# Performance work log

Hardware: AMD Instinct MI355X
Metric: run time of the kernel (lower is better)

Reference implementation:

```python
import jax, jax.numpy as jnp
import numpy as np

B, T, D = 16, 512, 256          # batch, seq_len, d_model (= num features = num graph nodes N)
H, MC, K, DE, DH = 4, 4, 3, 10, 128
GS, SS, AS = 4, 6, 4            # global/sector/asset regime states
TAU = 0.5
STEPS = 3                       # diffusion steps
HID = max(64, D)
DEC_H = max(64, D // 2)


def setup_inputs() -> dict:
    key = jax.random.key(0)
    ks = iter(jax.random.split(key, 64))

    def nrm(shape, s=0.02):
        return (s * jax.random.normal(next(ks), shape)).astype(jnp.float32)

    z = lambda *s: jnp.zeros(s, jnp.float32)
    o = lambda *s: jnp.ones(s, jnp.float32)
    p = dict(
        x=jax.random.normal(next(ks), (B, T, D), dtype=jnp.float32),
        # hierarchical regime controller
        gW1=nrm((D, HID)), gb1=z(HID), g_ln_w=o(HID), g_ln_b=z(HID),
        gW2=nrm((HID, GS)), gb2=z(GS),
        sW1=nrm((D, HID)), sb1=z(HID), sW2=nrm((HID, D * SS)), sb2=z(D * SS),
        aW1=nrm((D, HID)), ab1=z(HID), aW2=nrm((HID, D * AS)), ab2=z(D * AS),
        global_prior=z(GS), sector_prior=z(SS), asset_prior=z(AS),
        g2f=nrm((GS, D)),
        sector_emb=jax.random.normal(next(ks), (SS, D), dtype=jnp.float32),
        asset_emb=jax.random.normal(next(ks), (AS, D), dtype=jnp.float32),
        # bidirectional temporal scan (BI-Mamba stand-in)
        decay_f=nrm((D,), 1.0), decay_b=nrm((D,), 1.0),
        tW=nrm((D, D)), tb=z(D),
        # Bayesian MAGAC + diffusion graph prior
        psi=nrm((H, D, DE), 0.1), log_sigma=jnp.full((H,), -2.0, jnp.float32),
        step_logits=jnp.linspace(-1.0, 0.5, STEPS).astype(jnp.float32),
        noise_scale=jnp.full((STEPS,), 0.05, jnp.float32),
        Wk=nrm((K + 1, T, DH)),
        mean_w=nrm((DH,)), mean_b=z(), lv_w=nrm((DH,)), lv_b=z(),
        # risk-aware decoder
        dW1=nrm((D, DEC_H)), db1=z(DEC_H), d_ln_w=o(DEC_H), d_ln_b=z(DEC_H),
        mW=nrm((DEC_H,)), mb=z(), lvW=nrm((DEC_H,)), lvb=z(),
        cW=nrm((DEC_H,)), cb=z(),
    )
    return p


def _ln(h, w, b):
    m = h.mean(-1, keepdims=True)
    v = h.var(-1, keepdims=True)  # biased, matches torch LayerNorm
    return (h - m) / jnp.sqrt(v + 1e-5) * w + b


def _gelu(h):
    return jax.nn.gelu(h, approximate=False)


def _gumbel_softmax(k, logits):
    u = jax.random.uniform(k, logits.shape, minval=1e-6, maxval=1.0 - 1e-6)
    g = -jnp.log(-jnp.log(u))
    return jax.nn.softmax((logits + g) / TAU, axis=-1)


def _fwd(x, gW1, gb1, g_ln_w, g_ln_b, gW2, gb2, sW1, sb1, sW2, sb2,
         aW1, ab1, aW2, ab2, global_prior, sector_prior, asset_prior,
         g2f, sector_emb, asset_emb, decay_f, decay_b, tW, tb,
         psi, log_sigma, step_logits, noise_scale, Wk,
         mean_w, mean_b, lv_w, lv_b,
         dW1, db1, d_ln_w, d_ln_b, mW, mb, lvW, lvb, cW, cb):
    rk = jax.random.key(42)
    k_g, k_s, k_a, k_eps, k_diff = jax.random.split(rk, 5)

    # ---- hierarchical regime controller ----
    seq_mean = x.mean(1)                               # (B, D)
    diff_summary = (x[:, 1:] - x[:, :-1]).mean(1)      # (B, D)
    g_logits = _gelu(_ln(seq_mean @ gW1 + gb1, g_ln_w, g_ln_b)) @ gW2 + gb2
    s_logits = (_gelu(seq_mean @ sW1 + sb1) @ sW2 + sb2).reshape(B, D, SS)
    a_logits = (_gelu(diff_summary @ aW1 + ab1) @ aW2 + ab2).reshape(B, D, AS)
    g_probs = _gumbel_softmax(k_g, g_logits)
    s_probs = _gumbel_softmax(k_s, s_logits)
    a_probs = _gumbel_softmax(k_a, a_logits)
    global_gate = g_probs @ g2f                                   # (B, D)
    # diagonal of einsum('bfs,sd->bfd') == einsum('bfs,sf->bf')
    sector_gate = jnp.einsum('bfs,sf->bf', s_probs, sector_emb)
    asset_gate = jnp.einsum('bfs,sf->bf', a_probs, asset_emb)
    feature_gate = jax.nn.sigmoid(global_gate + sector_gate + asset_gate)
    gated_x = x * feature_gate[:, None, :]

    # ---- bidirectional temporal EMA scan (BI-Mamba stand-in) ----
    af = jax.nn.sigmoid(decay_f)
    abk = jax.nn.sigmoid(decay_b)
    xs = gated_x.transpose(1, 0, 2)                    # (T, B, D)

    def ema(a):
        def step(h, xt):
            h = a * h + (1.0 - a) * xt
            return h, h
        return step

    _, hf = jax.lax.scan(ema(af), jnp.zeros_like(xs[0]), xs)
    _, hb = jax.lax.scan(ema(abk), jnp.zeros_like(xs[0]), xs[::-1])
    temporal = (hf + hb[::-1]).transpose(1, 0, 2) @ tW + tb       # (B, T, D)
    node_major = temporal.transpose(0, 2, 1)                      # (B, N=D, T)

    # ---- Bayesian adjacency sampling (MC samples per head) ----
    logits = jnp.einsum('hne,hme->hnm', psi, psi) / jnp.sqrt(jnp.float32(DE))
    sigma = jnp.exp(log_sigma)                                    # (H,)
    eps = jax.random.normal(k_eps, (MC, H, D, D))
    A = jax.nn.softmax(logits[None] + sigma[None, :, None, None] * eps, axis=-1)

    # ---- diffusion refinement guided by regime features ----
    ctx = feature_gate.mean(0)
    ctx = ctx / (jnp.linalg.norm(ctx) + 1e-6)
    outer = ctx[:, None] * ctx[None, :]
    outer = outer / jnp.maximum(outer.sum(-1, keepdims=True), 1e-6)
    dkeys = jax.random.split(k_diff, STEPS)
    for s in range(STEPS):                             # fixed small loop, vectorized over (MC,H)
        alpha = jax.nn.sigmoid(step_logits[s])
        noise = noise_scale[s] * jax.random.normal(dkeys[s], A.shape)
        A = alpha * A + (1.0 - alpha) * outer + noise
        A = 0.5 * (A + jnp.swapaxes(A, -1, -2))
        A = jax.nn.softmax(A, axis=-1)

    # ---- K-hop graph conv, averaged over MC samples and heads ----
    Z = jnp.einsum('bnt,td->bnd', node_major, Wk[0])[None, None]  # hop 0
    P = jnp.broadcast_to(node_major, (MC, H, B, D, T))
    for k in range(1, K + 1):
        P = jnp.einsum('mhnp,mhbpt->mhbnt', A, P)
        Z = Z + jnp.einsum('mhbnt,td->mhbnd', P, Wk[k])
    Z = Z.mean((0, 1))                                            # (B, N, DH)
    graph_mean = Z @ mean_w + mean_b                              # (B, N)
    graph_logvar = Z @ lv_w + lv_b                                # (B, N)

    # ---- risk-aware decoder ----
    feat = _ln(_gelu(graph_mean @ dW1 + db1), d_ln_w, d_ln_b)     # (B, DEC_H)
    mean = feat @ mW + mb
    dec_logvar = feat @ lvW + lvb
    _cvar = jax.nn.sigmoid(feat @ cW + cb)  # auxiliary head (not in returned output)
    var = jnp.exp(dec_logvar) + jnp.exp(graph_logvar).sum(1)
    log_var = jnp.log(var)
    return jnp.stack([mean, log_var], axis=-1)                    # (B, 2)


def reference(x, gW1, gb1, g_ln_w, g_ln_b, gW2, gb2, sW1, sb1, sW2, sb2,
              aW1, ab1, aW2, ab2, global_prior, sector_prior, asset_prior,
              g2f, sector_emb, asset_emb, decay_f, decay_b, tW, tb,
              psi, log_sigma, step_logits, noise_scale, Wk,
              mean_w, mean_b, lv_w, lv_b,
              dW1, db1, d_ln_w, d_ln_b, mW, mb, lvW, lvb, cW, cb):
    return _fwd(x, gW1, gb1, g_ln_w, g_ln_b, gW2, gb2, sW1, sb1, sW2, sb2,
                aW1, ab1, aW2, ab2, global_prior, sector_prior, asset_prior,
                g2f, sector_emb, asset_emb, decay_f, decay_b, tW, tb,
                psi, log_sigma, step_logits, noise_scale, Wk,
                mean_w, mean_b, lv_w, lv_b,
                dW1, db1, d_ln_w, d_ln_b, mW, mb, lvW, lvb, cW, cb)
```

## Files before the change

### kernel.cpp

```cpp
#include <hip/hip_runtime.h>
#include <stdint.h>

#define PARTITIONABLE 1

namespace {

struct TFPair { uint32_t a, b; };

__host__ __device__ constexpr uint32_t rotl32(uint32_t x, int d) {
  return (x << d) | (x >> (32 - d));
}

__host__ __device__ constexpr TFPair tf2x32(uint32_t k0, uint32_t k1,
                                            uint32_t x0, uint32_t x1) {
  uint32_t k2 = k0 ^ k1 ^ 0x1BD11BDAu;
  x0 += k0; x1 += k1;
  x0 += x1; x1 = rotl32(x1, 13); x1 ^= x0;
  x0 += x1; x1 = rotl32(x1, 15); x1 ^= x0;
  x0 += x1; x1 = rotl32(x1, 26); x1 ^= x0;
  x0 += x1; x1 = rotl32(x1, 6);  x1 ^= x0;
  x0 += k1; x1 += k2 + 1u;
  x0 += x1; x1 = rotl32(x1, 17); x1 ^= x0;
  x0 += x1; x1 = rotl32(x1, 29); x1 ^= x0;
  x0 += x1; x1 = rotl32(x1, 16); x1 ^= x0;
  x0 += x1; x1 = rotl32(x1, 24); x1 ^= x0;
  x0 += k2; x1 += k0 + 2u;
  x0 += x1; x1 = rotl32(x1, 13); x1 ^= x0;
  x0 += x1; x1 = rotl32(x1, 15); x1 ^= x0;
  x0 += x1; x1 = rotl32(x1, 26); x1 ^= x0;
  x0 += x1; x1 = rotl32(x1, 6);  x1 ^= x0;
  x0 += k0; x1 += k1 + 3u;
  x0 += x1; x1 = rotl32(x1, 17); x1 ^= x0;
  x0 += x1; x1 = rotl32(x1, 29); x1 ^= x0;
  x0 += x1; x1 = rotl32(x1, 16); x1 ^= x0;
  x0 += x1; x1 = rotl32(x1, 24); x1 ^= x0;
  x0 += k1; x1 += k2 + 4u;
  x0 += x1; x1 = rotl32(x1, 13); x1 ^= x0;
  x0 += x1; x1 = rotl32(x1, 15); x1 ^= x0;
  x0 += x1; x1 = rotl32(x1, 26); x1 ^= x0;
  x0 += x1; x1 = rotl32(x1, 6);  x1 ^= x0;
  x0 += k2; x1 += k0 + 5u;
  return TFPair{x0, x1};
}

#if PARTITIONABLE
constexpr TFPair KG  = tf2x32(0u, 42u, 0u, 0u);
constexpr TFPair KS  = tf2x32(0u, 42u, 0u, 1u);
constexpr TFPair KA  = tf2x32(0u, 42u, 0u, 2u);
constexpr TFPair KE  = tf2x32(0u, 42u, 0u, 3u);
constexpr TFPair KD  = tf2x32(0u, 42u, 0u, 4u);
constexpr TFPair DK0 = tf2x32(KD.a, KD.b, 0u, 0u);
constexpr TFPair DK1 = tf2x32(KD.a, KD.b, 0u, 1u);
constexpr TFPair DK2 = tf2x32(KD.a, KD.b, 0u, 2u);
#else
constexpr TFPair SP0 = tf2x32(0u, 42u, 0u, 5u);
constexpr TFPair SP1 = tf2x32(0u, 42u, 1u, 6u);
constexpr TFPair SP2 = tf2x32(0u, 42u, 2u, 7u);
constexpr TFPair SP3 = tf2x32(0u, 42u, 3u, 8u);
constexpr TFPair SP4 = tf2x32(0u, 42u, 4u, 9u);
constexpr TFPair KG  = TFPair{SP0.a, SP1.a};
constexpr TFPair KS  = TFPair{SP2.a, SP3.a};
constexpr TFPair KA  = TFPair{SP4.a, SP0.b};
constexpr TFPair KE  = TFPair{SP1.b, SP2.b};
constexpr TFPair KD  = TFPair{SP3.b, SP4.b};
constexpr TFPair DP0 = tf2x32(KD.a, KD.b, 0u, 3u);
constexpr TFPair DP1 = tf2x32(KD.a, KD.b, 1u, 4u);
constexpr TFPair DP2 = tf2x32(KD.a, KD.b, 2u, 5u);
constexpr TFPair DK0 = TFPair{DP0.a, DP1.a};
constexpr TFPair DK1 = TFPair{DP2.a, DP0.b};
constexpr TFPair DK2 = TFPair{DP1.b, DP2.b};
#endif

__device__ __forceinline__ uint32_t rbits(uint32_t k0, uint32_t k1,
                                          uint32_t idx, uint32_t half) {
#if PARTITIONABLE
  TFPair t = tf2x32(k0, k1, 0u, idx);
  return t.a ^ t.b;
#else
  if (idx < half) return tf2x32(k0, k1, idx, idx + half).a;
  return tf2x32(k0, k1, idx - half, idx).b;
#endif
}

__device__ __forceinline__ float bits_to_u01(uint32_t bits) {
  return __uint_as_float((bits >> 9) | 0x3F800000u) - 1.0f;
}

__device__ __forceinline__ float gumbel_u(uint32_t k0, uint32_t k1,
                                          uint32_t idx, uint32_t half) {
  const float mn = 1e-6f;
  const float mx = 1.0f - 1e-6f;
  float f = bits_to_u01(rbits(k0, k1, idx, half));
  return fmaxf(mn, f * (mx - mn) + mn);
}

__device__ __forceinline__ float erfinv_f32(float x) {
  float w = -log1pf(-x * x);
  float p;
  if (w < 5.0f) {
    w -= 2.5f;
    p = 2.81022636e-08f;
    p = fmaf(p, w, 3.43273939e-07f);
    p = fmaf(p, w, -3.5233877e-06f);
    p = fmaf(p, w, -4.39150654e-06f);
    p = fmaf(p, w, 0.00021858087f);
    p = fmaf(p, w, -0.00125372503f);
    p = fmaf(p, w, -0.00417768164f);
    p = fmaf(p, w, 0.246640727f);
    p = fmaf(p, w, 1.50140941f);
  } else {
    w = sqrtf(w) - 3.0f;
    p = -0.000200214257f;
    p = fmaf(p, w, 0.000100950558f);
    p = fmaf(p, w, 0.00134934322f);
    p = fmaf(p, w, -0.00367342844f);
    p = fmaf(p, w, 0.00573950773f);
    p = fmaf(p, w, -0.0076224613f);
    p = fmaf(p, w, 0.00943887047f);
    p = fmaf(p, w, 1.00167406f);
    p = fmaf(p, w, 2.83297682f);
  }
  return p * x;
}

__device__ __forceinline__ float normal_from(uint32_t k0, uint32_t k1,
                                             uint32_t idx, uint32_t half) {
  const float lo = -0x1.fffffep-1f;
  float f = bits_to_u01(rbits(k0, k1, idx, half));
  float u = fmaxf(lo, f * 2.0f + lo);
  return 1.41421356237f * erfinv_f32(u);
}

__device__ __forceinline__ float gelu_f(float x) {
  return 0.5f * x * (1.0f + erff(x / 1.4142135623730951f));
}
__device__ __forceinline__ float sigmoid_f(float x) {
  return 1.0f / (1.0f + expf(-x));
}

__device__ __forceinline__ float wave_sum(float v) {
  #pragma unroll
  for (int m = 32; m > 0; m >>= 1) v += __shfl_xor(v, m);
  return v;
}
__device__ __forceinline__ float wave_max(float v) {
  #pragma unroll
  for (int m = 32; m > 0; m >>= 1) v = fmaxf(v, __shfl_xor(v, m));
  return v;
}
template <int NW>
__device__ __forceinline__ float blk_sum(float v, float* slots) {
  v = wave_sum(v);
  int wid = threadIdx.x >> 6;
  if ((threadIdx.x & 63) == 0) slots[wid] = v;
  __syncthreads();
  float r = slots[0];
  #pragma unroll
  for (int i = 1; i < NW; ++i) r += slots[i];
  return r;
}
template <int NW>
__device__ __forceinline__ float blk_max(float v, float* slots) {
  v = wave_max(v);
  int wid = threadIdx.x >> 6;
  if ((threadIdx.x & 63) == 0) slots[wid] = v;
  __syncthreads();
  float r = slots[0];
  #pragma unroll
  for (int i = 1; i < NW; ++i) r = fmaxf(r, slots[i]);
  return r;
}

struct Params {
  const float *x, *gW1, *gb1, *glnw, *glnb, *gW2, *gb2, *sW1, *sb1, *sW2, *sb2,
      *aW1, *ab1, *aW2, *ab2, *g2f, *semb, *aemb, *decay_f, *decay_b, *tW, *tb,
      *psi, *log_sigma, *step_logits, *noise_scale, *Wk, *mean_w, *mean_b,
      *lv_w, *lv_b, *dW1, *db1, *dlnw, *dlnb, *mW, *mb, *lvW, *lvb;
  float* out;
  float *fg, *ctx, *v, *sv, *u, *Pf, *Qf, *Pb, *Qb, *Lf, *Lb, *YH,
      *R1, *gm, *glv, *A, *A2, *At, *At2, *hgS, *hgA, *lvS, *lvA, *gpv;
};


__device__ __forceinline__ void phase_w1head(const Params& P, float* smem,
                                             int blk, int tid) {
  float* src  = smem;
  float* s1   = smem + 256;
  float* s2   = smem + 260;
  float* gsl  = smem + 264;
  float* gvals= smem + 280;
  int head = blk >> 4, b = blk & 15;
  const float* xb = P.x + (size_t)b * 512 * 256 + tid;
  if (head < 2) {
    float s = 0.f;
    for (int tc = 0; tc < 16; ++tc) {
      float ps = 0.f;
      #pragma unroll
      for (int i = 0; i < 32; ++i) ps += xb[(size_t)(tc * 32 + i) * 256];
      s += ps;
    }
    src[tid] = s / 512.0f;
  } else {
    src[tid] = (xb[(size_t)511 * 256] - xb[0]) / 511.0f;
  }
  __syncthreads();
  const float* W = (head == 0) ? P.gW1 : (head == 1) ? P.sW1 : P.aW1;
  const float* bias = (head == 0) ? P.gb1 : (head == 1) ? P.sb1 : P.ab1;
  float acc = bias[tid];
  #pragma unroll 8
  for (int d = 0; d < 256; ++d)
    acc = fmaf(src[d], W[(size_t)d * 256 + tid], acc);
  if (head == 1) { P.hgS[b * 256 + tid] = gelu_f(acc); return; }
  if (head == 2) { P.hgA[b * 256 + tid] = gelu_f(acc); return; }
  float mean = blk_sum<4>(acc, s1) / 256.0f;
  float dv = acc - mean;
  float var = blk_sum<4>(dv * dv, s2) / 256.0f;
  float hg = gelu_f(dv / sqrtf(var + 1e-5f) * P.glnw[tid] + P.glnb[tid]);
  float lg[4];
  #pragma unroll
  for (int sx = 0; sx < 4; ++sx)
    lg[sx] = blk_sum<4>(hg * P.gW2[tid * 4 + sx], gsl + 4 * sx);
  if (tid < 4) {
    float u = gumbel_u(KG.a, KG.b, (uint32_t)(b * 4 + tid), 32u);
    float g = -logf(-logf(u));
    gvals[tid] = (lg[tid] + P.gb2[tid] + g) / 0.5f;
  }
  __syncthreads();
  if (tid < 4) {
    float mx = fmaxf(fmaxf(gvals[0], gvals[1]), fmaxf(gvals[2], gvals[3]));
    float sum = expf(gvals[0] - mx) + expf(gvals[1] - mx) +
                expf(gvals[2] - mx) + expf(gvals[3] - mx);
    P.gpv[b * 4 + tid] = expf(gvals[tid] - mx) / sum;
  }
}

__device__ __forceinline__ void phase_l2gemm(const Params& P, float* smem,
                                             int blk, int tid) {
  float* h = smem;
  if (blk < 96) {
    int b = blk / 6, ct = blk % 6;
    h[tid] = P.hgS[b * 256 + tid];
    __syncthreads();
    int col = ct * 256 + tid;
    float acc = P.sb2[col];
    const float* wp = P.sW2 + col;
    #pragma unroll 8
    for (int d = 0; d < 256; ++d) acc = fmaf(h[d], wp[(size_t)d * 1536], acc);
    int f = col / 6, sx = col - f * 6;
    float u = gumbel_u(KS.a, KS.b, (uint32_t)(b * 256 + f) * 6u + sx, 12288u);
    P.lvS[b * 1536 + col] = (acc + (-logf(-logf(u)))) / 0.5f;
  } else {
    int idx = blk - 96;
    int b = idx >> 2, ct = idx & 3;
    h[tid] = P.hgA[b * 256 + tid];
    __syncthreads();
    int col = ct * 256 + tid;
    float acc = P.ab2[col];
    const float* wp = P.aW2 + col;
    #pragma unroll 8
    for (int d = 0; d < 256; ++d) acc = fmaf(h[d], wp[(size_t)d * 1024], acc);
    int f = col >> 2, sx = col & 3;
    float u = gumbel_u(KA.a, KA.b, (uint32_t)(b * 256 + f) * 4u + sx, 8192u);
    P.lvA[b * 1024 + col] = (acc + (-logf(-logf(u)))) / 0.5f;
  }
}

__device__ __forceinline__ void phase_gfin(const Params& P, int b, int tid) {
  int f = tid;
  const float* lvSb = P.lvS + b * 1536 + f * 6;
  float v0 = lvSb[0], v1 = lvSb[1], v2 = lvSb[2];
  float v3 = lvSb[3], v4 = lvSb[4], v5 = lvSb[5];
  float mx = fmaxf(fmaxf(fmaxf(v0, v1), fmaxf(v2, v3)), fmaxf(v4, v5));
  float e0 = expf(v0 - mx), e1 = expf(v1 - mx), e2 = expf(v2 - mx);
  float e3 = expf(v3 - mx), e4 = expf(v4 - mx), e5 = expf(v5 - mx);
  float ssum = e0 + e1 + e2 + e3 + e4 + e5;
  float sg = (e0 / ssum) * P.semb[0 * 256 + f] + (e1 / ssum) * P.semb[1 * 256 + f] +
             (e2 / ssum) * P.semb[2 * 256 + f] + (e3 / ssum) * P.semb[3 * 256 + f] +
             (e4 / ssum) * P.semb[4 * 256 + f] + (e5 / ssum) * P.semb[5 * 256 + f];
  const float* lvAb = P.lvA + b * 1024 + f * 4;
  float a0 = lvAb[0], a1 = lvAb[1], a2 = lvAb[2], a3 = lvAb[3];
  float amx = fmaxf(fmaxf(a0, a1), fmaxf(a2, a3));
  float x0 = expf(a0 - amx), x1 = expf(a1 - amx);
  float x2 = expf(a2 - amx), x3 = expf(a3 - amx);
  float asum = x0 + x1 + x2 + x3;
  float ag = (x0 / asum) * P.aemb[0 * 256 + f] + (x1 / asum) * P.aemb[1 * 256 + f] +
             (x2 / asum) * P.aemb[2 * 256 + f] + (x3 / asum) * P.aemb[3 * 256 + f];
  float gg = 0.f;
  #pragma unroll
  for (int sx = 0; sx < 4; ++sx) gg = fmaf(P.gpv[b * 4 + sx], P.g2f[sx * 256 + f], gg);
  P.fg[b * 256 + f] = sigmoid_f(gg + sg + ag);
}

__device__ __forceinline__ void phase_vcompute(const Params& P, int bid2,
                                               int tid) {
  int j = bid2 >> 2, tg = bid2 & 3;
  const float* wp = (j & 1) ? P.lv_w : P.mean_w;
  const float* Wkk = P.Wk + (size_t)(j >> 1) * 65536;
  int wid = tid >> 6, lane = tid & 63;
  float w0 = wp[lane], w1 = wp[64 + lane];
  float svloc = 0.f;
  for (int i = 0; i < 32; ++i) {
    int t = tg * 128 + wid * 32 + i;
    const float* row = Wkk + (size_t)t * 128;
    float s = row[lane] * w0 + row[64 + lane] * w1;
    s = wave_sum(s);
    if (lane == 0) { P.v[j * 512 + t] = s; svloc += s; }
  }
  if (lane == 0) P.sv[j * 16 + tg * 4 + wid] = svloc;
}

__device__ __forceinline__ void phase_ainit_row(const Params& P, float* smem,
                                                int blk, int tid) {
  float* pn = smem;
  float* s1 = smem + 12;
  float* s2 = smem + 16;
  int mh = blk >> 8, h = mh & 3, n = blk & 255, p = tid;
  if (p < 10) pn[p] = P.psi[(size_t)(h * 256 + n) * 10 + p];
  __syncthreads();
  const float* pp = P.psi + (size_t)(h * 256 + p) * 10;
  float s = 0.f;
  #pragma unroll
  for (int e = 0; e < 10; ++e) s = fmaf(pn[e], pp[e], s);
  float logit = s / sqrtf(10.0f);
  uint32_t idx = (uint32_t)blk * 256u + (uint32_t)p;
  float eps = normal_from(KE.a, KE.b, idx, 524288u);
  float val = logit + expf(P.log_sigma[h]) * eps;
  float mx = blk_max<4>(val, s1);
  float e = expf(val - mx);
  float sum = blk_sum<4>(e, s2);
  P.A[(size_t)blk * 256 + p] = e / sum;
}

__device__ __forceinline__ void phase_ctx(const Params& P, float* smem,
                                          int tid) {
  float* s1 = smem;
  float* s2 = smem + 4;
  float c = 0.f;
  for (int b = 0; b < 16; ++b) c += P.fg[b * 256 + tid];
  c /= 16.0f;
  float ss = blk_sum<4>(c * c, s1);
  float cv = c / (sqrtf(ss) + 1e-6f);
  P.ctx[tid] = cv;
  float S = blk_sum<4>(cv, s2);
  if (tid == 0) P.ctx[256] = S;
}

__device__ __forceinline__ void phase_transA(const Params& P, float* smem,
                                             int blk, int tid) {
  float* tile = smem;
  int mh = blk >> 6;
  int tr = ((blk >> 3) & 7) * 32, tc = (blk & 7) * 32;
  const float* src = P.A + (size_t)mh * 65536;
  float* dst = P.At + (size_t)mh * 65536;
  int lr = tid >> 5, lc = tid & 31;
  #pragma unroll
  for (int p = 0; p < 4; ++p) {
    int r = p * 8 + lr;
    tile[r * 33 + lc] = src[(size_t)(tr + r) * 256 + tc + lc];
  }
  __syncthreads();
  #pragma unroll
  for (int p = 0; p < 4; ++p) {
    int r = p * 8 + lr;
    dst[(size_t)(tc + r) * 256 + tr + lc] = tile[lc * 33 + r];
  }
}

__device__ __forceinline__ void phase_scan1(const Params& P, float* smem,
                                            int ch, int tid) {
  float* vv = smem;
  int b = ch >> 4, c = ch & 15;
  int d = tid;
  vv[(d >> 5) * 32 + (d & 31)] = P.v[(d >> 5) * 512 + c * 32 + (d & 31)];
  __syncthreads();
  float g = P.fg[b * 256 + d];
  float af = sigmoid_f(P.decay_f[d]);
  float ab = sigmoid_f(P.decay_b[d]);
  float r_gx[32];
  const float* xp = P.x + ((size_t)b * 512 + c * 32) * 256 + d;
  #pragma unroll
  for (int i = 0; i < 32; ++i) r_gx[i] = xp[(size_t)i * 256] * g;
  float h = 0.f, pw = 1.f;
  float Pr[8], Q[8];
  #pragma unroll
  for (int j = 0; j < 8; ++j) { Pr[j] = 0.f; Q[j] = 0.f; }
  #pragma unroll
  for (int i = 0; i < 32; ++i) {
    h = fmaf(af, h, (1.0f - af) * r_gx[i]);
    pw *= af;
    #pragma unroll
    for (int j = 0; j < 8; ++j) {
      float vj = vv[j * 32 + i];
      Pr[j] = fmaf(h, vj, Pr[j]);
      Q[j] = fmaf(pw, vj, Q[j]);
    }
  }
  size_t base = ((size_t)(b * 16 + c) * 8) * 256 + d;
  #pragma unroll
  for (int j = 0; j < 8; ++j) {
    P.Pf[base + j * 256] = Pr[j];
    P.Qf[base + j * 256] = Q[j];
  }
  P.Lf[(b * 16 + c) * 256 + d] = h;
  h = 0.f; pw = 1.f;
  #pragma unroll
  for (int j = 0; j < 8; ++j) { Pr[j] = 0.f; Q[j] = 0.f; }
  #pragma unroll
  for (int i = 31; i >= 0; --i) {
    h = fmaf(ab, h, (1.0f - ab) * r_gx[i]);
    pw *= ab;
    #pragma unroll
    for (int j = 0; j < 8; ++j) {
      float vj = vv[j * 32 + i];
      Pr[j] = fmaf(h, vj, Pr[j]);
      Q[j] = fmaf(pw, vj, Q[j]);
    }
  }
  #pragma unroll
  for (int j = 0; j < 8; ++j) {
    P.Pb[base + j * 256] = Pr[j];
    P.Qb[base + j * 256] = Q[j];
  }
  P.Lb[(b * 16 + c) * 256 + d] = h;
}

__device__ __forceinline__ void phase_scan2(const Params& P, int blk, int tid) {
  int b = blk >> 3, j = blk & 7;
  int d = tid;
  float af = sigmoid_f(P.decay_f[d]);
  float ab = sigmoid_f(P.decay_b[d]);
  float af32 = af, ab32 = ab;
  #pragma unroll
  for (int q = 0; q < 5; ++q) { af32 *= af32; ab32 *= ab32; }
  float acc = 0.f, H = 0.f;
  for (int c = 0; c < 16; ++c) {
    size_t base = ((size_t)(b * 16 + c) * 8 + j) * 256 + d;
    acc += P.Pf[base] + H * P.Qf[base];
    H = P.Lf[(b * 16 + c) * 256 + d] + af32 * H;
  }
  H = 0.f;
  for (int c = 15; c >= 0; --c) {
    size_t base = ((size_t)(b * 16 + c) * 8 + j) * 256 + d;
    acc += P.Pb[base] + H * P.Qb[base];
    H = P.Lb[(b * 16 + c) * 256 + d] + ab32 * H;
  }
  P.u[(b * 8 + j) * 256 + d] = acc;
}

__device__ __forceinline__ void phase_ygemm(const Params& P, float* smem,
                                            int blk32, int tid) {
  float* As = smem;
  float* Bs = smem + 1056;
  float* svs = smem + 2112;
  int n0 = (blk32 & 7) * 32, m0 = (blk32 >> 3) * 32;
  int tx = tid & 31, ty = tid >> 5;
  if (tid < 8) {
    float ssv = 0.f;
    #pragma unroll
    for (int q = 0; q < 16; ++q) ssv += P.sv[tid * 16 + q];
    svs[tid] = ssv;
  }
  float acc[4] = {0.f, 0.f, 0.f, 0.f};
  for (int k0 = 0; k0 < 256; k0 += 32) {
    #pragma unroll
    for (int l = 0; l < 4; ++l) {
      int e = tid + l * 256, r = e >> 5, cc = e & 31;
      As[r * 33 + cc] = P.u[(size_t)(m0 + r) * 256 + k0 + cc];
      Bs[r * 33 + cc] = P.tW[(size_t)(k0 + r) * 256 + n0 + cc];
    }
    __syncthreads();
    #pragma unroll
    for (int kk = 0; kk < 32; ++kk) {
      float bv = Bs[kk * 33 + tx];
      #pragma unroll
      for (int i = 0; i < 4; ++i)
        acc[i] = fmaf(As[(ty + 8 * i) * 33 + kk], bv, acc[i]);
    }
    __syncthreads();
  }
  int n = n0 + tx;
  float tbn = P.tb[n];
  float mb0 = P.mean_b[0], lb0 = P.lv_b[0];
  #pragma unroll
  for (int i = 0; i < 4; ++i) {
    int row = m0 + ty + 8 * i;
    int b = row >> 3, j = row & 7;
    float val = acc[i] + tbn * svs[j];
    if (j == 0) P.gm[b * 256 + n] = val + mb0;
    else if (j == 1) P.glv[b * 256 + n] = val + lb0;
    else {
      int k = (j >> 1) - 1, proj = j & 1;
      P.YH[k * 8192 + n * 32 + b * 2 + proj] = val;
    }
  }
}

template <bool WRITE_T>
__device__ __forceinline__ void phase_mix4(const Params& P, float* smem,
                                           int sidx, const float* Ain,
                                           const float* AinT, float* Aout,
                                           float* AoutT, uint32_t dk0,
                                           uint32_t dk1, int blk, int tid) {
  float* vals = smem;
  float* slots = smem + 4 * 257;
  int mh = blk >> 6, r0 = (blk & 63) * 4;
  float alpha = sigmoid_f(P.step_logits[sidx]);
  float ns = P.noise_scale[sidx];
  float S = P.ctx[256];
  int c = tid;
  float cp = P.ctx[c];
  const size_t mbase = (size_t)mh * 65536;
  #pragma unroll
  for (int r = 0; r < 4; ++r) {
    int n = r0 + r;
    float cn = P.ctx[n];
    float o_np = (cn * cp) / fmaxf(cn * S, 1e-6f);
    float o_pn = (cp * cn) / fmaxf(cp * S, 1e-6f);
    uint32_t i_np = (uint32_t)(mh * 65536 + n * 256 + c);
    uint32_t i_pn = (uint32_t)(mh * 65536 + c * 256 + n);
    float a_np = Ain[mbase + (size_t)n * 256 + c];
    float a_pn = AinT[mbase + (size_t)n * 256 + c];
    float m_np = alpha * a_np + (1.0f - alpha) * o_np +
                 ns * normal_from(dk0, dk1, i_np, 524288u);
    float m_pn = alpha * a_pn + (1.0f - alpha) * o_pn +
                 ns * normal_from(dk0, dk1, i_pn, 524288u);
    vals[r * 257 + c] = 0.5f * (m_np + m_pn);
  }
  __syncthreads();
  #pragma unroll
  for (int r = 0; r < 4; ++r) {
    float val = vals[r * 257 + c];
    float mx = blk_max<4>(val, slots + r * 8);
    float e = expf(val - mx);
    float sum = blk_sum<4>(e, slots + r * 8 + 4);
    float o = e / sum;
    Aout[mbase + (size_t)(r0 + r) * 256 + c] = o;
    if (WRITE_T) vals[r * 257 + c] = o;
  }
  if (WRITE_T) {
    __syncthreads();
    float t0 = vals[0 * 257 + c], t1 = vals[1 * 257 + c];
    float t2 = vals[2 * 257 + c], t3 = vals[3 * 257 + c];
    float4* dst = (float4*)(AoutT + mbase + (size_t)c * 256 + r0);
    dst[0] = make_float4(t0, t1, t2, t3);
  }
}

__device__ __forceinline__ void phase_findec(const Params& P, float* smem,
                                             int bid, int tid) {
  float* gmv = smem;
  float* sl = smem + 256;
  int b = bid;
  float sm_ = 0.f, sl_ = 0.f;
  for (int mh = 0; mh < 16; ++mh) {
    sm_ += P.R1[(size_t)mh * 8192 + tid * 32 + b * 2];
    sl_ += P.R1[(size_t)mh * 8192 + tid * 32 + b * 2 + 1];
  }
  float gmn = P.gm[b * 256 + tid] + sm_ * (1.0f / 16.0f);
  float gln = P.glv[b * 256 + tid] + sl_ * (1.0f / 16.0f);
  gmv[tid] = gmn;
  float se = expf(gln);
  __syncthreads();
  float sumexp = blk_sum<4>(se, sl);
  float h = 0.f;
  if (tid < 128) {
    h = P.db1[tid];
    for (int n = 0; n < 256; ++n) h = fmaf(gmv[n], P.dW1[n * 128 + tid], h);
    h = gelu_f(h);
  }
  float mean = blk_sum<4>(tid < 128 ? h : 0.f, sl + 4) / 128.0f;
  float dv = (tid < 128) ? h - mean : 0.f;
  float var = blk_sum<4>(dv * dv, sl + 8) / 128.0f;
  float feat = (tid < 128) ? dv / sqrtf(var + 1e-5f) * P.dlnw[tid] + P.dlnb[tid]
                           : 0.f;
  float m_c = blk_sum<4>(tid < 128 ? feat * P.mW[tid] : 0.f, sl + 12) + P.mb[0];
  float lv_c = blk_sum<4>(tid < 128 ? feat * P.lvW[tid] : 0.f, sl + 16) + P.lvb[0];
  if (tid == 0) {
    P.out[b * 2 + 0] = m_c;
    P.out[b * 2 + 1] = logf(expf(lv_c) + sumexp);
  }
}


__global__ __launch_bounds__(256) void kA(Params P) {
  __shared__ float smem[288];
  int bid = blockIdx.x, tid = threadIdx.x;
  if (bid < 48) phase_w1head(P, smem, bid, tid);
  else if (bid < 80) phase_vcompute(P, bid - 48, tid);
  else phase_ainit_row(P, smem, bid - 80, tid);
}

__global__ __launch_bounds__(256) void kL2(Params P) {
  __shared__ float smem[1056];
  int bid = blockIdx.x, tid = threadIdx.x;
  if (bid < 160) phase_l2gemm(P, smem, bid, tid);
  else phase_transA(P, smem, bid - 160, tid);
}

__global__ __launch_bounds__(256) void kGF(Params P) {
  __shared__ float smem[1056];
  int bid = blockIdx.x, tid = threadIdx.x;
  if (bid < 16) phase_gfin(P, bid, tid);
  else phase_transA(P, smem, bid - 16 + 512, tid);
}

__global__ __launch_bounds__(256) void kScan(Params P) {
  __shared__ float smem[256];
  int bid = blockIdx.x, tid = threadIdx.x;
  if (bid < 256) phase_scan1(P, smem, bid, tid);
  else phase_ctx(P, smem, tid);
}

__global__ __launch_bounds__(256) void kM0(Params P) {
  __shared__ float smem[1060];
  int bid = blockIdx.x, tid = threadIdx.x;
  if (bid < 1024)
    phase_mix4<true>(P, smem, 0, P.A, P.At, P.A2, P.At2, DK0.a, DK0.b, bid, tid);
  else
    phase_scan2(P, bid - 1024, tid);
}

__global__ __launch_bounds__(256) void kM1(Params P) {
  __shared__ float smem[2120];
  int bid = blockIdx.x, tid = threadIdx.x;
  if (bid < 1024)
    phase_mix4<true>(P, smem, 1, P.A2, P.At2, P.A, P.At, DK1.a, DK1.b, bid, tid);
  else
    phase_ygemm(P, smem, bid - 1024, tid);
}

__global__ __launch_bounds__(256) void kM2(Params P) {
  __shared__ float smem[1060];
  phase_mix4<false>(P, smem, 2, P.A, P.At, P.A2, nullptr, DK2.a, DK2.b,
                    blockIdx.x, threadIdx.x);
}

__global__ __launch_bounds__(256) void kHor(Params P) {
  __shared__ float Rc[512];
  int bid = blockIdx.x, tid = threadIdx.x;
  int mh = bid >> 4, c0 = (bid & 15) * 2;
  const float* Ab = P.A2 + (size_t)mh * 65536;
  const float4* Arow = (const float4*)(Ab + (size_t)tid * 256);
  const float* Y2 = P.YH + 2 * 8192;
  Rc[tid * 2 + 0] = Y2[tid * 32 + c0 + 0];
  Rc[tid * 2 + 1] = Y2[tid * 32 + c0 + 1];
  __syncthreads();
  #pragma unroll
  for (int hop = 0; hop < 3; ++hop) {
    float acc0 = 0.f, acc1 = 0.f;
    const float4* Rc4 = (const float4*)Rc;
    for (int k4 = 0; k4 < 64; ++k4) {
      float4 a = Arow[k4];
      float4 r01 = Rc4[k4 * 2];
      float4 r23 = Rc4[k4 * 2 + 1];
      acc0 = fmaf(a.x, r01.x, acc0); acc1 = fmaf(a.x, r01.y, acc1);
      acc0 = fmaf(a.y, r01.z, acc0); acc1 = fmaf(a.y, r01.w, acc1);
      acc0 = fmaf(a.z, r23.x, acc0); acc1 = fmaf(a.z, r23.y, acc1);
      acc0 = fmaf(a.w, r23.z, acc0); acc1 = fmaf(a.w, r23.w, acc1);
    }
    if (hop == 0) {
      acc0 += P.YH[8192 + tid * 32 + c0 + 0];
      acc1 += P.YH[8192 + tid * 32 + c0 + 1];
    } else if (hop == 1) {
      acc0 += P.YH[tid * 32 + c0 + 0];
      acc1 += P.YH[tid * 32 + c0 + 1];
    }
    __syncthreads();
    Rc[tid * 2 + 0] = acc0;
    Rc[tid * 2 + 1] = acc1;
    __syncthreads();
  }
  P.R1[(size_t)mh * 8192 + (size_t)tid * 32 + c0 + 0] = Rc[tid * 2 + 0];
  P.R1[(size_t)mh * 8192 + (size_t)tid * 32 + c0 + 1] = Rc[tid * 2 + 1];
}

__global__ __launch_bounds__(256) void kFin(Params P) {
  __shared__ float smem[276];
  phase_findec(P, smem, blockIdx.x, threadIdx.x);
}

constexpr size_t O_FG = 0;
constexpr size_t O_CTX = 4096;
constexpr size_t O_V = 4480;
constexpr size_t O_SV = 8576;
constexpr size_t O_U = 8704;
constexpr size_t O_PF = 41472;
constexpr size_t O_QF = 565760;
constexpr size_t O_PB = 1090048;
constexpr size_t O_QB = 1614336;
constexpr size_t O_LF = 2138624;
constexpr size_t O_LB = 2204160;
constexpr size_t O_YH = 2269696;
constexpr size_t O_R1 = 2294272;
constexpr size_t O_GM = 2425344;
constexpr size_t O_GLV = 2429440;
constexpr size_t O_A = 2433536;
constexpr size_t O_A2 = 3482112;
constexpr size_t O_AT = 4530688;
constexpr size_t O_AT2 = 5579264;
constexpr size_t O_HGS = 6627840;
constexpr size_t O_HGA = 6631936;
constexpr size_t O_LVS = 6636032;
constexpr size_t O_LVA = 6660608;
constexpr size_t O_GPV = 6676992;

}

extern "C" void kernel_launch(void* const* d_in, const int* in_sizes, int n_in,
                              void* d_out, int out_size, void* d_ws,
                              size_t ws_size, hipStream_t stream) {
  (void)in_sizes; (void)n_in; (void)out_size; (void)ws_size;
  float* w = (float*)d_ws;
  Params prm;
  prm.x = (const float*)d_in[0];
  prm.gW1 = (const float*)d_in[1];
  prm.gb1 = (const float*)d_in[2];
  prm.glnw = (const float*)d_in[3];
  prm.glnb = (const float*)d_in[4];
  prm.gW2 = (const float*)d_in[5];
  prm.gb2 = (const float*)d_in[6];
  prm.sW1 = (const float*)d_in[7];
  prm.sb1 = (const float*)d_in[8];
  prm.sW2 = (const float*)d_in[9];
  prm.sb2 = (const float*)d_in[10];
  prm.aW1 = (const float*)d_in[11];
  prm.ab1 = (const float*)d_in[12];
  prm.aW2 = (const float*)d_in[13];
  prm.ab2 = (const float*)d_in[14];
  prm.g2f = (const float*)d_in[18];
  prm.semb = (const float*)d_in[19];
  prm.aemb = (const float*)d_in[20];
  prm.decay_f = (const float*)d_in[21];
  prm.decay_b = (const float*)d_in[22];
  prm.tW = (const float*)d_in[23];
  prm.tb = (const float*)d_in[24];
  prm.psi = (const float*)d_in[25];
  prm.log_sigma = (const float*)d_in[26];
  prm.step_logits = (const float*)d_in[27];
  prm.noise_scale = (const float*)d_in[28];
  prm.Wk = (const float*)d_in[29];
  prm.mean_w = (const float*)d_in[30];
  prm.mean_b = (const float*)d_in[31];
  prm.lv_w = (const float*)d_in[32];
  prm.lv_b = (const float*)d_in[33];
  prm.dW1 = (const float*)d_in[34];
  prm.db1 = (const float*)d_in[35];
  prm.dlnw = (const float*)d_in[36];
  prm.dlnb = (const float*)d_in[37];
  prm.mW = (const float*)d_in[38];
  prm.mb = (const float*)d_in[39];
  prm.lvW = (const float*)d_in[40];
  prm.lvb = (const float*)d_in[41];
  prm.out = (float*)d_out;
  prm.fg = w + O_FG;
  prm.ctx = w + O_CTX;
  prm.v = w + O_V;
  prm.sv = w + O_SV;
  prm.u = w + O_U;
  prm.Pf = w + O_PF;
  prm.Qf = w + O_QF;
  prm.Pb = w + O_PB;
  prm.Qb = w + O_QB;
  prm.Lf = w + O_LF;
  prm.Lb = w + O_LB;
  prm.YH = w + O_YH;
  prm.R1 = w + O_R1;
  prm.gm = w + O_GM;
  prm.glv = w + O_GLV;
  prm.A = w + O_A;
  prm.A2 = w + O_A2;
  prm.At = w + O_AT;
  prm.At2 = w + O_AT2;
  prm.hgS = w + O_HGS;
  prm.hgA = w + O_HGA;
  prm.lvS = w + O_LVS;
  prm.lvA = w + O_LVA;
  prm.gpv = w + O_GPV;

  kA<<<4176, 256, 0, stream>>>(prm);
  kL2<<<672, 256, 0, stream>>>(prm);
  kGF<<<528, 256, 0, stream>>>(prm);
  kScan<<<257, 256, 0, stream>>>(prm);
  kM0<<<1152, 256, 0, stream>>>(prm);
  kM1<<<1056, 256, 0, stream>>>(prm);
  kM2<<<1024, 256, 0, stream>>>(prm);
  kHor<<<256, 256, 0, stream>>>(prm);
  kFin<<<16, 256, 0, stream>>>(prm);
}
```

Measured before the change: 294.6 us.

## Fuse regime gate GEMM with softmax gating, drop kGF launch, widen Horner tiles

Result: slower. 306.0 us (+3.9%).

```diff
diff --git a/kernel.cpp b/kernel.cpp
--- a/kernel.cpp
+++ b/kernel.cpp
@@ -178,7 +178,7 @@
       *lv_w, *lv_b, *dW1, *db1, *dlnw, *dlnb, *mW, *mb, *lvW, *lvb;
   float* out;
   float *fg, *ctx, *v, *sv, *u, *Pf, *Qf, *Pb, *Qb, *Lf, *Lb, *YH,
-      *R1, *gm, *glv, *A, *A2, *At, *At2, *hgS, *hgA, *lvS, *lvA, *gpv;
+      *R1, *gm, *glv, *A, *A2, *At, *At2, *hgS, *hgA, *gpv;
 };
 
 
@@ -234,61 +234,73 @@
   }
 }
 
-__device__ __forceinline__ void phase_l2gemm(const Params& P, float* smem,
+__device__ __forceinline__ void phase_l2gate(const Params& P, float* smem,
                                              int blk, int tid) {
-  float* h = smem;
-  if (blk < 96) {
-    int b = blk / 6, ct = blk % 6;
-    h[tid] = P.hgS[b * 256 + tid];
-    __syncthreads();
-    int col = ct * 256 + tid;
-    float acc = P.sb2[col];
-    const float* wp = P.sW2 + col;
-    #pragma unroll 8
-    for (int d = 0; d < 256; ++d) acc = fmaf(h[d], wp[(size_t)d * 1536], acc);
-    int f = col / 6, sx = col - f * 6;
+  float* hS  = smem;
+  float* hA  = smem + 256;
+  float* lvS = smem + 512;
+  float* lvA = smem + 896;
+  int b = blk >> 2, f0 = (blk & 3) * 64;
+  hS[tid] = P.hgS[b * 256 + tid];
+  hA[tid] = P.hgA[b * 256 + tid];
+  __syncthreads();
+  int colA = f0 * 4 + tid;
+  int colS0 = f0 * 6 + tid;
+  int colS1 = f0 * 6 + 256 + (tid & 127);
+  float accA = P.ab2[colA];
+  float accS0 = P.sb2[colS0];
+  float accS1 = P.sb2[colS1];
+  const float* wpA = P.aW2 + colA;
+  const float* wpS0 = P.sW2 + colS0;
+  const float* wpS1 = P.sW2 + colS1;
+  #pragma unroll 4
+  for (int d = 0; d < 256; ++d) {
+    float ha = hA[d], hs = hS[d];
+    accA = fmaf(ha, wpA[(size_t)d * 1024], accA);
+    accS0 = fmaf(hs, wpS0[(size_t)d * 1536], accS0);
+    accS1 = fmaf(hs, wpS1[(size_t)d * 1536], accS1);
+  }
+  {
+    int f = colA >> 2, sx = colA & 3;
+    float u = gumbel_u(KA.a, KA.b, (uint32_t)(b * 256 + f) * 4u + sx, 8192u);
+    lvA[tid] = (accA + (-logf(-logf(u)))) / 0.5f;
+  }
+  {
+    int f = colS0 / 6, sx = colS0 - f * 6;
     float u = gumbel_u(KS.a, KS.b, (uint32_t)(b * 256 + f) * 6u + sx, 12288u);
-    P.lvS[b * 1536 + col] = (acc + (-logf(-logf(u)))) / 0.5f;
-  } else {
-    int idx = blk - 96;
-    int b = idx >> 2, ct = idx & 3;
-    h[tid] = P.hgA[b * 256 + tid];
-    __syncthreads();
-    int col = ct * 256 + tid;
-    float acc = P.ab2[col];
-    const float* wp = P.aW2 + col;
-    #pragma unroll 8
-    for (int d = 0; d < 256; ++d) acc = fmaf(h[d], wp[(size_t)d * 1024], acc);
-    int f = col >> 2, sx = col & 3;
-    float u = gumbel_u(KA.a, KA.b, (uint32_t)(b * 256 + f) * 4u + sx, 8192u);
-    P.lvA[b * 1024 + col] = (acc + (-logf(-logf(u)))) / 0.5f;
-  }
-}
-
-__device__ __forceinline__ void phase_gfin(const Params& P, int b, int tid) {
-  int f = tid;
-  const float* lvSb = P.lvS + b * 1536 + f * 6;
-  float v0 = lvSb[0], v1 = lvSb[1], v2 = lvSb[2];
-  float v3 = lvSb[3], v4 = lvSb[4], v5 = lvSb[5];
-  float mx = fmaxf(fmaxf(fmaxf(v0, v1), fmaxf(v2, v3)), fmaxf(v4, v5));
-  float e0 = expf(v0 - mx), e1 = expf(v1 - mx), e2 = expf(v2 - mx);
-  float e3 = expf(v3 - mx), e4 = expf(v4 - mx), e5 = expf(v5 - mx);
-  float ssum = e0 + e1 + e2 + e3 + e4 + e5;
-  float sg = (e0 / ssum) * P.semb[0 * 256 + f] + (e1 / ssum) * P.semb[1 * 256 + f] +
-             (e2 / ssum) * P.semb[2 * 256 + f] + (e3 / ssum) * P.semb[3 * 256 + f] +
-             (e4 / ssum) * P.semb[4 * 256 + f] + (e5 / ssum) * P.semb[5 * 256 + f];
-  const float* lvAb = P.lvA + b * 1024 + f * 4;
-  float a0 = lvAb[0], a1 = lvAb[1], a2 = lvAb[2], a3 = lvAb[3];
-  float amx = fmaxf(fmaxf(a0, a1), fmaxf(a2, a3));
-  float x0 = expf(a0 - amx), x1 = expf(a1 - amx);
-  float x2 = expf(a2 - amx), x3 = expf(a3 - amx);
-  float asum = x0 + x1 + x2 + x3;
-  float ag = (x0 / asum) * P.aemb[0 * 256 + f] + (x1 / asum) * P.aemb[1 * 256 + f] +
-             (x2 / asum) * P.aemb[2 * 256 + f] + (x3 / asum) * P.aemb[3 * 256 + f];
-  float gg = 0.f;
-  #pragma unroll
-  for (int sx = 0; sx < 4; ++sx) gg = fmaf(P.gpv[b * 4 + sx], P.g2f[sx * 256 + f], gg);
-  P.fg[b * 256 + f] = sigmoid_f(gg + sg + ag);
+    lvS[tid] = (accS0 + (-logf(-logf(u)))) / 0.5f;
+  }
+  if (tid < 128) {
+    int f = colS1 / 6, sx = colS1 - f * 6;
+    float u = gumbel_u(KS.a, KS.b, (uint32_t)(b * 256 + f) * 6u + sx, 12288u);
+    lvS[256 + tid] = (accS1 + (-logf(-logf(u)))) / 0.5f;
+  }
+  __syncthreads();
+  if (tid < 64) {
+    int f = f0 + tid;
+    float v0 = lvS[tid * 6 + 0], v1 = lvS[tid * 6 + 1], v2 = lvS[tid * 6 + 2];
+    float v3 = lvS[tid * 6 + 3], v4 = lvS[tid * 6 + 4], v5 = lvS[tid * 6 + 5];
+    float mx = fmaxf(fmaxf(fmaxf(v0, v1), fmaxf(v2, v3)), fmaxf(v4, v5));
+    float e0 = expf(v0 - mx), e1 = expf(v1 - mx), e2 = expf(v2 - mx);
+    float e3 = expf(v3 - mx), e4 = expf(v4 - mx), e5 = expf(v5 - mx);
+    float ssum = e0 + e1 + e2 + e3 + e4 + e5;
+    float sg = (e0 / ssum) * P.semb[0 * 256 + f] + (e1 / ssum) * P.semb[1 * 256 + f] +
+               (e2 / ssum) * P.semb[2 * 256 + f] + (e3 / ssum) * P.semb[3 * 256 + f] +
+               (e4 / ssum) * P.semb[4 * 256 + f] + (e5 / ssum) * P.semb[5 * 256 + f];
+    float a0 = lvA[tid * 4 + 0], a1 = lvA[tid * 4 + 1];
+    float a2 = lvA[tid * 4 + 2], a3 = lvA[tid * 4 + 3];
+    float amx = fmaxf(fmaxf(a0, a1), fmaxf(a2, a3));
+    float x0 = expf(a0 - amx), x1 = expf(a1 - amx);
+    float x2 = expf(a2 - amx), x3 = expf(a3 - amx);
+    float asum = x0 + x1 + x2 + x3;
+    float ag = (x0 / asum) * P.aemb[0 * 256 + f] + (x1 / asum) * P.aemb[1 * 256 + f] +
+               (x2 / asum) * P.aemb[2 * 256 + f] + (x3 / asum) * P.aemb[3 * 256 + f];
+    float gg = 0.f;
+    #pragma unroll
+    for (int sx = 0; sx < 4; ++sx)
+      gg = fmaf(P.gpv[b * 4 + sx], P.g2f[sx * 256 + f], gg);
+    P.fg[b * 256 + f] = sigmoid_f(gg + sg + ag);
+  }
 }
 
 __device__ __forceinline__ void phase_vcompute(const Params& P, int bid2,
@@ -510,6 +522,7 @@
   int c = tid;
   float cp = P.ctx[c];
   const size_t mbase = (size_t)mh * 65536;
+  float vr[4];
   #pragma unroll
   for (int r = 0; r < 4; ++r) {
     int n = r0 + r;
@@ -524,26 +537,89 @@
                  ns * normal_from(dk0, dk1, i_np, 524288u);
     float m_pn = alpha * a_pn + (1.0f - alpha) * o_pn +
                  ns * normal_from(dk0, dk1, i_pn, 524288u);
-    vals[r * 257 + c] = 0.5f * (m_np + m_pn);
-  }
-  __syncthreads();
+    vr[r] = 0.5f * (m_np + m_pn);
+  }
+  int wid = tid >> 6, lane = tid & 63;
+  float wm[4];
+  #pragma unroll
+  for (int r = 0; r < 4; ++r) wm[r] = wave_max(vr[r]);
+  if (lane == 0) {
+    #pragma unroll
+    for (int r = 0; r < 4; ++r) slots[r * 8 + wid] = wm[r];
+  }
+  __syncthreads();
+  float er[4];
   #pragma unroll
   for (int r = 0; r < 4; ++r) {
-    float val = vals[r * 257 + c];
-    float mx = blk_max<4>(val, slots + r * 8);
-    float e = expf(val - mx);
-    float sum = blk_sum<4>(e, slots + r * 8 + 4);
-    float o = e / sum;
-    Aout[mbase + (size_t)(r0 + r) * 256 + c] = o;
-    if (WRITE_T) vals[r * 257 + c] = o;
+    float mx = slots[r * 8 + 0];
+    #pragma unroll
+    for (int i = 1; i < 4; ++i) mx = fmaxf(mx, slots[r * 8 + i]);
+    er[r] = expf(vr[r] - mx);
+  }
+  float ws[4];
+  #pragma unroll
+  for (int r = 0; r < 4; ++r) ws[r] = wave_sum(er[r]);
+  if (lane == 0) {
+    #pragma unroll
+    for (int r = 0; r < 4; ++r) slots[r * 8 + 4 + wid] = ws[r];
+  }
+  __syncthreads();
+  float orow[4];
+  #pragma unroll
+  for (int r = 0; r < 4; ++r) {
+    float sum = slots[r * 8 + 4 + 0];
+    #pragma unroll
+    for (int i = 1; i < 4; ++i) sum += slots[r * 8 + 4 + i];
+    orow[r] = er[r] / sum;
+    Aout[mbase + (size_t)(r0 + r) * 256 + c] = orow[r];
   }
   if (WRITE_T) {
+    float4* dst = (float4*)(AoutT + mbase + (size_t)c * 256 + r0);
+    dst[0] = make_float4(orow[0], orow[1], orow[2], orow[3]);
+  }
+}
+
+__device__ __forceinline__ void phase_horner8(const Params& P, int bid,
+                                              int tid, float* Rc) {
+  int mh = bid >> 2, c0 = (bid & 3) * 8;
+  const float* Ab = P.A2 + (size_t)mh * 65536;
+  const float4* Arow = (const float4*)(Ab + (size_t)tid * 256);
+  const float* Y2 = P.YH + 2 * 8192;
+  #pragma unroll
+  for (int j = 0; j < 8; ++j) Rc[tid * 8 + j] = Y2[tid * 32 + c0 + j];
+  __syncthreads();
+  #pragma unroll
+  for (int hop = 0; hop < 3; ++hop) {
+    float acc[8];
+    #pragma unroll
+    for (int j = 0; j < 8; ++j) acc[j] = 0.f;
+    for (int k4 = 0; k4 < 64; ++k4) {
+      float4 a = Arow[k4];
+      const float* r0p = Rc + (k4 * 4) * 8;
+      #pragma unroll
+      for (int j = 0; j < 8; ++j) acc[j] = fmaf(a.x, r0p[j], acc[j]);
+      #pragma unroll
+      for (int j = 0; j < 8; ++j) acc[j] = fmaf(a.y, r0p[8 + j], acc[j]);
+      #pragma unroll
+      for (int j = 0; j < 8; ++j) acc[j] = fmaf(a.z, r0p[16 + j], acc[j]);
+      #pragma unroll
+      for (int j = 0; j < 8; ++j) acc[j] = fmaf(a.w, r0p[24 + j], acc[j]);
+    }
+    if (hop == 0) {
+      #pragma unroll
+      for (int j = 0; j < 8; ++j) acc[j] += P.YH[8192 + tid * 32 + c0 + j];
+    } else if (hop == 1) {
+      #pragma unroll
+      for (int j = 0; j < 8; ++j) acc[j] += P.YH[tid * 32 + c0 + j];
+    }
     __syncthreads();
-    float t0 = vals[0 * 257 + c], t1 = vals[1 * 257 + c];
-    float t2 = vals[2 * 257 + c], t3 = vals[3 * 257 + c];
-    float4* dst = (float4*)(AoutT + mbase + (size_t)c * 256 + r0);
-    dst[0] = make_float4(t0, t1, t2, t3);
-  }
+    #pragma unroll
+    for (int j = 0; j < 8; ++j) Rc[tid * 8 + j] = acc[j];
+    __syncthreads();
+  }
+  #pragma unroll
+  for (int j = 0; j < 8; ++j)
+    P.R1[(size_t)mh * 8192 + (size_t)(c0 + j) * 256 + tid] = Rc[tid * 8 + j];
 }
 
 __device__ __forceinline__ void phase_findec(const Params& P, float* smem,
@@ -553,8 +629,8 @@
   int b = bid;
   float sm_ = 0.f, sl_ = 0.f;
   for (int mh = 0; mh < 16; ++mh) {
-    sm_ += P.R1[(size_t)mh * 8192 + tid * 32 + b * 2];
-    sl_ += P.R1[(size_t)mh * 8192 + tid * 32 + b * 2 + 1];
+    sm_ += P.R1[(size_t)mh * 8192 + (size_t)(b * 2) * 256 + tid];
+    sl_ += P.R1[(size_t)mh * 8192 + (size_t)(b * 2 + 1) * 256 + tid];
   }
   float gmn = P.gm[b * 256 + tid] + sm_ * (1.0f / 16.0f);
   float gln = P.glv[b * 256 + tid] + sl_ * (1.0f / 16.0f);
@@ -565,6 +641,7 @@
   float h = 0.f;
   if (tid < 128) {
     h = P.db1[tid];
+    #pragma unroll 8
     for (int n = 0; n < 256; ++n) h = fmaf(gmv[n], P.dW1[n * 128 + tid], h);
     h = gelu_f(h);
   }
@@ -591,17 +668,10 @@
 }
 
 __global__ __launch_bounds__(256) void kL2(Params P) {
-  __shared__ float smem[1056];
+  __shared__ float smem[1152];
   int bid = blockIdx.x, tid = threadIdx.x;
-  if (bid < 160) phase_l2gemm(P, smem, bid, tid);
-  else phase_transA(P, smem, bid - 160, tid);
-}
-
-__global__ __launch_bounds__(256) void kGF(Params P) {
-  __shared__ float smem[1056];
-  int bid = blockIdx.x, tid = threadIdx.x;
-  if (bid < 16) phase_gfin(P, bid, tid);
-  else phase_transA(P, smem, bid - 16 + 512, tid);
+  if (bid < 64) phase_l2gate(P, smem, bid, tid);
+  else phase_transA(P, smem, bid - 64, tid);
 }
 
 __global__ __launch_bounds__(256) void kScan(Params P) {
@@ -636,42 +706,8 @@
 }
 
 __global__ __launch_bounds__(256) void kHor(Params P) {
-  __shared__ float Rc[512];
-  int bid = blockIdx.x, tid = threadIdx.x;
-  int mh = bid >> 4, c0 = (bid & 15) * 2;
-  const float* Ab = P.A2 + (size_t)mh * 65536;
-  const float4* Arow = (const float4*)(Ab + (size_t)tid * 256);
-  const float* Y2 = P.YH + 2 * 8192;
-  Rc[tid * 2 + 0] = Y2[tid * 32 + c0 + 0];
-  Rc[tid * 2 + 1] = Y2[tid * 32 + c0 + 1];
-  __syncthreads();
-  #pragma unroll
-  for (int hop = 0; hop < 3; ++hop) {
-    float acc0 = 0.f, acc1 = 0.f;
-    const float4* Rc4 = (const float4*)Rc;
-    for (int k4 = 0; k4 < 64; ++k4) {
-      float4 a = Arow[k4];
-      float4 r01 = Rc4[k4 * 2];
-      float4 r23 = Rc4[k4 * 2 + 1];
-      acc0 = fmaf(a.x, r01.x, acc0); acc1 = fmaf(a.x, r01.y, acc1);
-      acc0 = fmaf(a.y, r01.z, acc0); acc1 = fmaf(a.y, r01.w, acc1);
-      acc0 = fmaf(a.z, r23.x, acc0); acc1 = fmaf(a.z, r23.y, acc1);
-      acc0 = fmaf(a.w, r23.z, acc0); acc1 = fmaf(a.w, r23.w, acc1);
-    }
-    if (hop == 0) {
-      acc0 += P.YH[8192 + tid * 32 + c0 + 0];
-      acc1 += P.YH[8192 + tid * 32 + c0 + 1];
-    } else if (hop == 1) {
-      acc0 += P.YH[tid * 32 + c0 + 0];
-      acc1 += P.YH[tid * 32 + c0 + 1];
-    }
-    __syncthreads();
-    Rc[tid * 2 + 0] = acc0;
-    Rc[tid * 2 + 1] = acc1;
-    __syncthreads();
-  }
-  P.R1[(size_t)mh * 8192 + (size_t)tid * 32 + c0 + 0] = Rc[tid * 2 + 0];
-  P.R1[(size_t)mh * 8192 + (size_t)tid * 32 + c0 + 1] = Rc[tid * 2 + 1];
+  __shared__ float Rc[2048];
+  phase_horner8(P, blockIdx.x, threadIdx.x, Rc);
 }
 
 __global__ __launch_bounds__(256) void kFin(Params P) {
@@ -700,9 +736,7 @@
 constexpr size_t O_AT2 = 5579264;
 constexpr size_t O_HGS = 6627840;
 constexpr size_t O_HGA = 6631936;
-constexpr size_t O_LVS = 6636032;
-constexpr size_t O_LVA = 6660608;
-constexpr size_t O_GPV = 6676992;
+constexpr size_t O_GPV = 6636032;
 
 }
 
@@ -773,17 +807,14 @@
   prm.At2 = w + O_AT2;
   prm.hgS = w + O_HGS;
   prm.hgA = w + O_HGA;
-  prm.lvS = w + O_LVS;
-  prm.lvA = w + O_LVA;
   prm.gpv = w + O_GPV;
 
   kA<<<4176, 256, 0, stream>>>(prm);
-  kL2<<<672, 256, 0, stream>>>(prm);
-  kGF<<<528, 256, 0, stream>>>(prm);
+  kL2<<<1088, 256, 0, stream>>>(prm);
   kScan<<<257, 256, 0, stream>>>(prm);
   kM0<<<1152, 256, 0, stream>>>(prm);
   kM1<<<1056, 256, 0, stream>>>(prm);
   kM2<<<1024, 256, 0, stream>>>(prm);
-  kHor<<<256, 256, 0, stream>>>(prm);
+  kHor<<<64, 256, 0, stream>>>(prm);
   kFin<<<16, 256, 0, stream>>>(prm);
 }
```
